# Kernel tuning notes

Measured on AMD Instinct MI355X. Metric: run time of the kernel, lower is better.

## Reference

```python
import jax, jax.numpy as jnp
import numpy as np
import math

N_HEADS = 16
ROPE_THETA = 10000.0


def _rope_cos_sin(seqlen, head_dim, theta=ROPE_THETA):
    # freqs_cis = polar(1, outer(t, 1/theta^(2i/d))) -> return cos, sin parts
    inv = 1.0 / (theta ** (jnp.arange(0, head_dim, 2, dtype=jnp.float32) / head_dim))
    t = jnp.arange(seqlen, dtype=jnp.float32)
    freqs = t[:, None] * inv[None, :]          # [S, hd/2]
    return jnp.cos(freqs), jnp.sin(freqs)


def _apply_rope(x, cos, sin):
    # x: [B, S, H, hd]; treat consecutive pairs as complex, rotate by e^{i*freq}
    B, S, H, hd = x.shape
    x2 = x.astype(jnp.float32).reshape(B, S, H, hd // 2, 2)
    xr, xi = x2[..., 0], x2[..., 1]
    c = cos[None, :, None, :]
    s = sin[None, :, None, :]
    out_r = xr * c - xi * s
    out_i = xr * s + xi * c
    return jnp.stack([out_r, out_i], axis=-1).reshape(B, S, H, hd).astype(x.dtype)


def setup_inputs() -> dict:
    key = jax.random.key(0)
    ks = jax.random.split(key, 5)
    dim = 2048
    B, S = 2, 2048
    scale = 1.0 / math.sqrt(dim)
    x = jax.random.normal(ks[0], (B, S, dim), dtype=jnp.float32)
    wq = jax.random.normal(ks[1], (dim, dim), dtype=jnp.float32) * scale
    wk = jax.random.normal(ks[2], (dim, dim), dtype=jnp.float32) * scale
    wv = jax.random.normal(ks[3], (dim, dim), dtype=jnp.float32) * scale
    wo = jax.random.normal(ks[4], (dim, dim), dtype=jnp.float32) * scale
    return {"x": x, "wq": wq, "wk": wk, "wv": wv, "wo": wo}


def reference(x, wq, wk, wv, wo):
    B, S, D = x.shape
    H = N_HEADS
    hd = D // H
    # nn.Linear(bias=False): y = x @ W.T
    q = (x @ wq.T).reshape(B, S, H, hd)
    k = (x @ wk.T).reshape(B, S, H, hd)
    v = (x @ wv.T).reshape(B, S, H, hd)
    cos, sin = _rope_cos_sin(S, hd)
    q = _apply_rope(q, cos, sin)
    k = _apply_rope(k, cos, sin)
    attn = jnp.einsum('bthd,bThd->bhtT', q, k) / jnp.sqrt(jnp.float32(hd))
    attn = jax.nn.softmax(attn, axis=-1)
    out = jnp.einsum('bhtT,bThd->bthd', attn, v).reshape(B, S, D)
    return out @ wo.T
```

## Files before the change

### kernel.cpp

```cpp
#include <hip/hip_runtime.h>
#include <math.h>

typedef unsigned short u16;
typedef __bf16 bf16x8 __attribute__((ext_vector_type(8)));
typedef short s16x4 __attribute__((ext_vector_type(4)));
typedef short s16x8 __attribute__((ext_vector_type(8)));
typedef float f32x4 __attribute__((ext_vector_type(4)));

#define B_ 2
#define S_ 2048
#define D_ 2048
#define H_ 16
#define HD_ 128
#define M_ 4096
#define N3_ 6144

#define AS1(p) ((__attribute__((address_space(1))) void*)(void*)(p))
#define AS3(p) ((__attribute__((address_space(3))) void*)(p))
#define GLD16(g, l) __builtin_amdgcn_global_load_lds(AS1(g), AS3(l), 16, 0, 0)

__device__ __forceinline__ u16 f2bf(float f) {
  unsigned u = __float_as_uint(f);
  return (u16)((u + 0x7FFFu + ((u >> 16) & 1u)) >> 16);
}
__device__ __forceinline__ float bf2f(u16 v) {
  return __uint_as_float(((unsigned)v) << 16);
}

__global__ void prep_k(const float* __restrict__ x, const float* __restrict__ wq,
                       const float* __restrict__ wk, const float* __restrict__ wv,
                       const float* __restrict__ wo, u16* __restrict__ xb,
                       u16* __restrict__ wqkvb, u16* __restrict__ wob,
                       float2* __restrict__ tab) {
  int idx = blockIdx.x * 256 + threadIdx.x;
  if (idx < 6291456) {
    const float* src;
    u16* dst;
    if (idx < 2097152) {
      src = x + (size_t)idx * 4;
      dst = xb + (size_t)idx * 4;
    } else if (idx < 5242880) {
      int ow = idx - 2097152;
      const float* w = ow < 1048576 ? wq : (ow < 2097152 ? wk : wv);
      int wo_off = ow & 1048575;
      src = w + (size_t)wo_off * 4;
      dst = wqkvb + (size_t)ow * 4;
    } else {
      int ow = idx - 5242880;
      src = wo + (size_t)ow * 4;
      dst = wob + (size_t)ow * 4;
    }
    float4 v = *(const float4*)src;
    ushort4 o;
    o.x = f2bf(v.x); o.y = f2bf(v.y); o.z = f2bf(v.z); o.w = f2bf(v.w);
    *(ushort4*)dst = o;
  } else {
    int t = idx - 6291456;
    int s = t >> 6, i = t & 63;
    double inv = exp2(-(double)i * (13.287712379549449 / 64.0));
    double fr = (double)s * inv;
    double sv, cv;
    sincos(fr, &sv, &cv);
    tab[t] = make_float2((float)cv, (float)sv);
  }
}

template <typename OT>
__global__ __launch_bounds__(256) void gemm_bt_k(const u16* __restrict__ A,
                                                 const u16* __restrict__ B,
                                                 OT* __restrict__ C,
                                                 int M, int N, int K) {
  __shared__ alignas(16) u16 As[128 * 32];
  __shared__ alignas(16) u16 Bs[128 * 32];
  const int tid = threadIdx.x;
  const int wave = tid >> 6, lane = tid & 63;
  const int quad = lane >> 4, l16 = lane & 15;
  const int m0 = blockIdx.y * 128, n0 = blockIdx.x * 128;
  const int wm = (wave >> 1) * 64, wn = (wave & 1) * 64;
  const u16* Ag = A + (size_t)m0 * K;
  const u16* Bg = B + (size_t)n0 * K;
  f32x4 acc[4][4] = {};
  const int c0 = tid, c1 = tid + 256;
  const int r0 = c0 >> 2, k0b = (c0 & 3) * 8;
  const int r1 = c1 >> 2, k1b = (c1 & 3) * 8;
  u16* la0 = As + (size_t)(wave * 64) * 8;
  u16* la1 = As + (size_t)(256 + wave * 64) * 8;
  u16* lb0 = Bs + (size_t)(wave * 64) * 8;
  u16* lb1 = Bs + (size_t)(256 + wave * 64) * 8;
  for (int kt = 0; kt < K; kt += 32) {
    GLD16(Ag + (size_t)r0 * K + kt + k0b, la0);
    GLD16(Ag + (size_t)r1 * K + kt + k1b, la1);
    GLD16(Bg + (size_t)r0 * K + kt + k0b, lb0);
    GLD16(Bg + (size_t)r1 * K + kt + k1b, lb1);
    __syncthreads();
    bf16x8 af[4], bfr[4];
#pragma unroll
    for (int i = 0; i < 4; ++i)
      af[i] = *(const bf16x8*)&As[(wm + i * 16 + l16) * 32 + quad * 8];
#pragma unroll
    for (int j = 0; j < 4; ++j)
      bfr[j] = *(const bf16x8*)&Bs[(wn + j * 16 + l16) * 32 + quad * 8];
#pragma unroll
    for (int i = 0; i < 4; ++i)
#pragma unroll
      for (int j = 0; j < 4; ++j)
        acc[i][j] = __builtin_amdgcn_mfma_f32_16x16x32_bf16(af[i], bfr[j], acc[i][j], 0, 0, 0);
    __syncthreads();
  }
#pragma unroll
  for (int i = 0; i < 4; ++i) {
#pragma unroll
    for (int j = 0; j < 4; ++j) {
      int n = n0 + wn + j * 16 + l16;
#pragma unroll
      for (int r = 0; r < 4; ++r) {
        int m = m0 + wm + i * 16 + quad * 4 + r;
        if constexpr (sizeof(OT) == 4)
          C[(size_t)m * N + n] = acc[i][j][r];
        else
          C[(size_t)m * N + n] = f2bf(acc[i][j][r]);
      }
    }
  }
}

__global__ void rv_k(const u16* __restrict__ qkv, const float2* __restrict__ tab,
                     u16* __restrict__ Qr, u16* __restrict__ Kr, u16* __restrict__ Vp) {
  int idx = blockIdx.x * 256 + threadIdx.x;
  if (idx < 4194304) {
    int m = idx >> 10;
    int h = (idx >> 6) & 15;
    int i = idx & 63;
    int s = m & (S_ - 1);
    int b = m >> 11;
    float2 cs = tab[(s << 6) | i];
    const u16* qp = qkv + (size_t)m * N3_ + h * HD_ + 2 * i;
    ushort2 qv = *(const ushort2*)qp;
    ushort2 kv = *(const ushort2*)(qp + D_);
    float qr = bf2f(qv.x), qi = bf2f(qv.y);
    float kr = bf2f(kv.x), ki = bf2f(kv.y);
    ushort2 qo, ko;
    qo.x = f2bf(qr * cs.x - qi * cs.y);
    qo.y = f2bf(qr * cs.y + qi * cs.x);
    ko.x = f2bf(kr * cs.x - ki * cs.y);
    ko.y = f2bf(kr * cs.y + ki * cs.x);
    size_t o = ((size_t)(b * H_ + h) * S_ + s) * HD_ + 2 * i;
    *(ushort2*)(Qr + o) = qo;
    *(ushort2*)(Kr + o) = ko;
  } else {
    int u = idx - 4194304;
    int bh = u >> 16, t = u & 65535;
    int b = bh >> 4, h = bh & 15;
    int d = t & 127, g = t >> 7;
    const u16* src = qkv + ((size_t)(b * S_ + 4 * g)) * N3_ + 2 * D_ + h * HD_ + d;
    ushort4 o;
    o.x = src[0];
    o.y = src[N3_];
    o.z = src[2 * N3_];
    o.w = src[3 * N3_];
    *(ushort4*)(Vp + (size_t)bh * S_ * HD_ + (size_t)t * 4) = o;
  }
}

#if __has_builtin(__builtin_amdgcn_mfma_f32_16x16x16bf16_1k)
#define HAS_MFMA16 1
#endif

__global__ __launch_bounds__(256, 3) void flash_k(const u16* __restrict__ Q,
                                                  const u16* __restrict__ Kc,
                                                  const u16* __restrict__ Vp,
                                                  float* __restrict__ Op0,
                                                  float* __restrict__ Op1,
                                                  float* __restrict__ lbuf) {
  __shared__ alignas(16) u16 sm[16384];
  u16* Ks = sm;
  u16* Vs = sm + 8192;
  const int tid = threadIdx.x;
  const int wave = tid >> 6, lane = tid & 63;
  const int quad = lane >> 4, l16 = lane & 15;
  const int qt = blockIdx.x;
  const int bh = blockIdx.y & 31, split = blockIdx.y >> 5;
  const int b = bh >> 4, h = bh & 15;

  bf16x8 qf[2][4];
#pragma unroll
  for (int half = 0; half < 2; ++half) {
#pragma unroll
    for (int i = 0; i < 4; ++i) {
      int c = i * 256 + tid, row = c >> 4, jl = c & 15;
      int gj = (jl & 8) | ((jl ^ row) & 7);
      GLD16(Q + ((size_t)bh * S_ + qt * 128 + half * 64 + row) * HD_ + gj * 8,
            sm + (size_t)(i * 256 + wave * 64) * 8);
    }
    __syncthreads();
    if ((wave >> 1) == half) {
      int wrow = (wave & 1) * 32;
#pragma unroll
      for (int qs = 0; qs < 2; ++qs) {
        int row = wrow + qs * 16 + l16;
#pragma unroll
        for (int dk = 0; dk < 4; ++dk) {
          int c = dk * 4 + quad, pj = (c & 8) | ((c ^ row) & 7);
          qf[qs][dk] = *(const bf16x8*)&sm[row * 128 + pj * 8];
        }
      }
    }
    __syncthreads();
  }

  f32x4 acco[2][8] = {};
  f32x4 accl[2] = {};
  const float SCL = 0.08838834764831845f * 1.4426950408889634f;
#ifdef HAS_MFMA16
  const s16x4 ones = {(short)0x3F80, (short)0x3F80, (short)0x3F80, (short)0x3F80};
#else
  union { s16x8 s; bf16x8 b; } onesu;
  onesu.s = (s16x8){(short)0x3F80, (short)0x3F80, (short)0x3F80, (short)0x3F80,
                    (short)0x3F80, (short)0x3F80, (short)0x3F80, (short)0x3F80};
#endif

  const int kt0 = split * 16, kt1 = kt0 + 16;
#pragma unroll 1
  for (int kt = kt0; kt < kt1; ++kt) {
#pragma unroll
    for (int i = 0; i < 4; ++i) {
      int c = i * 256 + tid, row = c >> 4, jl = c & 15;
      int gj = (jl & 8) | ((jl ^ row) & 7);
      GLD16(Kc + ((size_t)bh * S_ + kt * 64 + row) * HD_ + gj * 8,
            Ks + (size_t)(i * 256 + wave * 64) * 8);
    }
    const u16* vg = Vp + (size_t)bh * S_ * HD_ + (size_t)kt * 8192;
#pragma unroll
    for (int i = 0; i < 4; ++i)
      GLD16(vg + (size_t)(i * 256 + tid) * 8, Vs + (size_t)(i * 256 + wave * 64) * 8);
    __syncthreads();

    f32x4 sc[2][4] = {};
#pragma unroll
    for (int k4 = 0; k4 < 4; ++k4) {
      int row = k4 * 16 + l16;
#pragma unroll
      for (int dk = 0; dk < 4; ++dk) {
        int c = dk * 4 + quad, pj = (c & 8) | ((c ^ row) & 7);
        bf16x8 kf = *(const bf16x8*)&Ks[row * 128 + pj * 8];
        sc[0][k4] = __builtin_amdgcn_mfma_f32_16x16x32_bf16(kf, qf[0][dk], sc[0][k4], 0, 0, 0);
        sc[1][k4] = __builtin_amdgcn_mfma_f32_16x16x32_bf16(kf, qf[1][dk], sc[1][k4], 0, 0, 0);
      }
    }

#ifdef HAS_MFMA16
    s16x4 ap[2][4];
#else
    bf16x8 ap[2][4];
#endif
#pragma unroll
    for (int qs = 0; qs < 2; ++qs) {
#pragma unroll
      for (int k4 = 0; k4 < 4; ++k4) {
        f32x4 s = sc[qs][k4];
        u16 p0 = f2bf(__builtin_amdgcn_exp2f(s[0] * SCL));
        u16 p1 = f2bf(__builtin_amdgcn_exp2f(s[1] * SCL));
        u16 p2 = f2bf(__builtin_amdgcn_exp2f(s[2] * SCL));
        u16 p3 = f2bf(__builtin_amdgcn_exp2f(s[3] * SCL));
#ifdef HAS_MFMA16
        ap[qs][k4] = (s16x4){(short)p0, (short)p1, (short)p2, (short)p3};
#else
        union { s16x8 s8; bf16x8 b8; } u;
        u.s8 = (s16x8){(short)p0, (short)p1, (short)p2, (short)p3, 0, 0, 0, 0};
        ap[qs][k4] = u.b8;
#endif
      }
    }

#pragma unroll
    for (int ck = 0; ck < 4; ++ck) {
      int vbase = (ck * 4 + quad) * 512 + l16 * 4;
#pragma unroll
      for (int df = 0; df < 8; ++df) {
        s16x4 bv = *(const s16x4*)&Vs[vbase + df * 64];
#ifdef HAS_MFMA16
        acco[0][df] = __builtin_amdgcn_mfma_f32_16x16x16bf16_1k(ap[0][ck], bv, acco[0][df], 0, 0, 0);
        acco[1][df] = __builtin_amdgcn_mfma_f32_16x16x16bf16_1k(ap[1][ck], bv, acco[1][df], 0, 0, 0);
#else
        union { s16x8 s8; bf16x8 b8; } vb;
        vb.s8 = (s16x8){bv[0], bv[1], bv[2], bv[3], 0, 0, 0, 0};
        acco[0][df] = __builtin_amdgcn_mfma_f32_16x16x32_bf16(ap[0][ck], vb.b8, acco[0][df], 0, 0, 0);
        acco[1][df] = __builtin_amdgcn_mfma_f32_16x16x32_bf16(ap[1][ck], vb.b8, acco[1][df], 0, 0, 0);
#endif
      }
#ifdef HAS_MFMA16
      accl[0] = __builtin_amdgcn_mfma_f32_16x16x16bf16_1k(ones, ap[0][ck], accl[0], 0, 0, 0);
      accl[1] = __builtin_amdgcn_mfma_f32_16x16x16bf16_1k(ones, ap[1][ck], accl[1], 0, 0, 0);
#else
      accl[0] = __builtin_amdgcn_mfma_f32_16x16x32_bf16(onesu.b, ap[0][ck], accl[0], 0, 0, 0);
      accl[1] = __builtin_amdgcn_mfma_f32_16x16x32_bf16(onesu.b, ap[1][ck], accl[1], 0, 0, 0);
#endif
    }
    __syncthreads();
  }

  float* op = split ? Op1 : Op0;
#pragma unroll
  for (int qs = 0; qs < 2; ++qs) {
    int rowb = qt * 128 + wave * 32 + qs * 16 + quad * 4;
#pragma unroll
    for (int df = 0; df < 8; ++df) {
      int col = h * HD_ + df * 16 + l16;
#pragma unroll
      for (int r = 0; r < 4; ++r)
        op[((size_t)(b * S_ + rowb + r)) * D_ + col] = acco[qs][df][r];
    }
    if (quad == 0)
      lbuf[(size_t)split * 65536 + bh * 2048 + qt * 128 + wave * 32 + qs * 16 + l16] =
          accl[qs][0];
  }
}

__global__ void merge_k(const float* __restrict__ Op0, const float* __restrict__ Op1,
                        const float* __restrict__ lbuf, u16* __restrict__ Ob) {
  int i4 = blockIdx.x * 256 + threadIdx.x;
  int row = i4 >> 9, col4 = i4 & 511;
  int b = row >> 11, s = row & 2047, h4 = col4 >> 5;
  int bh = (b << 4) | h4;
  float l = lbuf[bh * 2048 + s] + lbuf[65536 + bh * 2048 + s];
  float inv = 1.0f / l;
  float4 a = ((const float4*)Op0)[i4];
  float4 c = ((const float4*)Op1)[i4];
  ushort4 o;
  o.x = f2bf((a.x + c.x) * inv);
  o.y = f2bf((a.y + c.y) * inv);
  o.z = f2bf((a.z + c.z) * inv);
  o.w = f2bf((a.w + c.w) * inv);
  ((ushort4*)Ob)[i4] = o;
}

extern "C" void kernel_launch(void* const* d_in, const int* in_sizes, int n_in,
                              void* d_out, int out_size, void* d_ws, size_t ws_size,
                              hipStream_t stream) {
  const float* x  = (const float*)d_in[0];
  const float* wq = (const float*)d_in[1];
  const float* wk = (const float*)d_in[2];
  const float* wv = (const float*)d_in[3];
  const float* wo = (const float*)d_in[4];

  size_t off = 0;
  char* ws = (char*)d_ws;
  u16* xb    = (u16*)(ws + off); off += (size_t)M_ * D_ * 2;
  u16* wqkvb = (u16*)(ws + off); off += (size_t)3 * D_ * D_ * 2;
  u16* wob   = (u16*)(ws + off); off += (size_t)D_ * D_ * 2;
  u16* qkv   = (u16*)(ws + off); off += (size_t)M_ * N3_ * 2;
  u16* Qr    = (u16*)(ws + off); off += (size_t)M_ * D_ * 2;
  u16* Kr    = (u16*)(ws + off); off += (size_t)M_ * D_ * 2;
  u16* Vp    = (u16*)(ws + off); off += (size_t)M_ * D_ * 2;
  float2* tab = (float2*)(ws + off); off += (size_t)S_ * 64 * sizeof(float2);
  float* Op0  = (float*)ws;
  u16*   Ob   = qkv;
  float* Op1  = (float*)(ws + ((size_t)64 << 20));
  float* lbuf = (float*)tab;
  if (off > ws_size) return;

  prep_k<<<25088, 256, 0, stream>>>(x, wq, wk, wv, wo, xb, wqkvb, wob, tab);
  gemm_bt_k<u16><<<dim3(N3_ / 128, M_ / 128), 256, 0, stream>>>(xb, wqkvb, qkv, M_, N3_, D_);
  rv_k<<<24576, 256, 0, stream>>>(qkv, tab, Qr, Kr, Vp);
  flash_k<<<dim3(S_ / 128, 64), 256, 0, stream>>>(Qr, Kr, Vp, Op0, Op1, lbuf);
  merge_k<<<(M_ * D_ / 4) / 256, 256, 0, stream>>>(Op0, Op1, lbuf, Ob);
  gemm_bt_k<float><<<dim3(D_ / 128, M_ / 128), 256, 0, stream>>>(Ob, wob, (float*)d_out, M_, D_, D_);
}
```

Baseline: 462.7 us.

## Fuse RoPE and V repack into QKV GEMM epilogue; drop flash split-K merge

The QKV GEMM now applies RoPE to Q and K and writes V in its packed layout directly from the accumulators, using a lane shuffle to pair neighbouring elements. This removes the separate rv_k pass and the bf16 qkv intermediate round trip through memory. Flash attention no longer splits the key range in two. Each block processes all 32 key tiles and normalizes in the epilogue, writing bf16 output directly, which removes merge_k and the two fp32 partial output buffers. The trade-off is half as many flash blocks (512 instead of 1024), so there is less parallelism to fill the GPU. The GEMM epilogue also adds scattered table loads.

```diff
diff --git a/kernel.cpp b/kernel.cpp
--- a/kernel.cpp
+++ b/kernel.cpp
@@ -62,6 +62,93 @@
     double sv, cv;
     sincos(fr, &sv, &cv);
     tab[t] = make_float2((float)cv, (float)sv);
+  }
+}
+
+__global__ __launch_bounds__(256) void gemm_qkv_k(const u16* __restrict__ A,
+                                                  const u16* __restrict__ B,
+                                                  const float2* __restrict__ tab,
+                                                  u16* __restrict__ Qr,
+                                                  u16* __restrict__ Kr,
+                                                  u16* __restrict__ Vp) {
+  __shared__ alignas(16) u16 As[128 * 32];
+  __shared__ alignas(16) u16 Bs[128 * 32];
+  const int K = D_;
+  const int tid = threadIdx.x;
+  const int wave = tid >> 6, lane = tid & 63;
+  const int quad = lane >> 4, l16 = lane & 15;
+  const int m0 = blockIdx.y * 128, n0 = blockIdx.x * 128;
+  const int wm = (wave >> 1) * 64, wn = (wave & 1) * 64;
+  const u16* Ag = A + (size_t)m0 * K;
+  const u16* Bg = B + (size_t)n0 * K;
+  f32x4 acc[4][4] = {};
+  const int c0 = tid, c1 = tid + 256;
+  const int r0 = c0 >> 2, k0b = (c0 & 3) * 8;
+  const int r1 = c1 >> 2, k1b = (c1 & 3) * 8;
+  u16* la0 = As + (size_t)(wave * 64) * 8;
+  u16* la1 = As + (size_t)(256 + wave * 64) * 8;
+  u16* lb0 = Bs + (size_t)(wave * 64) * 8;
+  u16* lb1 = Bs + (size_t)(256 + wave * 64) * 8;
+  for (int kt = 0; kt < K; kt += 32) {
+    GLD16(Ag + (size_t)r0 * K + kt + k0b, la0);
+    GLD16(Ag + (size_t)r1 * K + kt + k1b, la1);
+    GLD16(Bg + (size_t)r0 * K + kt + k0b, lb0);
+    GLD16(Bg + (size_t)r1 * K + kt + k1b, lb1);
+    __syncthreads();
+    bf16x8 af[4], bfr[4];
+#pragma unroll
+    for (int i = 0; i < 4; ++i)
+      af[i] = *(const bf16x8*)&As[(wm + i * 16 + l16) * 32 + quad * 8];
+#pragma unroll
+    for (int j = 0; j < 4; ++j)
+      bfr[j] = *(const bf16x8*)&Bs[(wn + j * 16 + l16) * 32 + quad * 8];
+#pragma unroll
+    for (int i = 0; i < 4; ++i)
+#pragma unroll
+      for (int j = 0; j < 4; ++j)
+        acc[i][j] = __builtin_amdgcn_mfma_f32_16x16x32_bf16(af[i], bfr[j], acc[i][j], 0, 0, 0);
+    __syncthreads();
+  }
+
+  const int region = n0 >> 11;
+  const int h = (n0 >> 7) & 15;
+  if (region < 2) {
+    u16* dst = region ? Kr : Qr;
+#pragma unroll
+    for (int i = 0; i < 4; ++i) {
+#pragma unroll
+      for (int j = 0; j < 4; ++j) {
+        int d = wn + j * 16 + l16;
+        int ii = d >> 1;
+        float sgn = (d & 1) ? 1.f : -1.f;
+#pragma unroll
+        for (int r = 0; r < 4; ++r) {
+          int m = m0 + wm + i * 16 + quad * 4 + r;
+          int s = m & (S_ - 1), b = m >> 11;
+          float2 cs = tab[(s << 6) + ii];
+          float v = acc[i][j][r];
+          float p = __shfl_xor(v, 1);
+          float o = v * cs.x + sgn * p * cs.y;
+          dst[((size_t)((b << 4) + h) * S_ + s) * HD_ + d] = f2bf(o);
+        }
+      }
+    }
+  } else {
+#pragma unroll
+    for (int i = 0; i < 4; ++i) {
+#pragma unroll
+      for (int j = 0; j < 4; ++j) {
+        int d = wn + j * 16 + l16;
+        int rowb = m0 + wm + i * 16 + quad * 4;
+        int b = rowb >> 11, sl = rowb & (S_ - 1);
+        ushort4 o;
+        o.x = f2bf(acc[i][j][0]);
+        o.y = f2bf(acc[i][j][1]);
+        o.z = f2bf(acc[i][j][2]);
+        o.w = f2bf(acc[i][j][3]);
+        *(ushort4*)(Vp + (size_t)((b << 4) + h) * S_ * HD_ + (size_t)(sl >> 2) * 512 + d * 4) = o;
+      }
+    }
   }
 }
 
@@ -124,44 +211,6 @@
   }
 }
 
-__global__ void rv_k(const u16* __restrict__ qkv, const float2* __restrict__ tab,
-                     u16* __restrict__ Qr, u16* __restrict__ Kr, u16* __restrict__ Vp) {
-  int idx = blockIdx.x * 256 + threadIdx.x;
-  if (idx < 4194304) {
-    int m = idx >> 10;
-    int h = (idx >> 6) & 15;
-    int i = idx & 63;
-    int s = m & (S_ - 1);
-    int b = m >> 11;
-    float2 cs = tab[(s << 6) | i];
-    const u16* qp = qkv + (size_t)m * N3_ + h * HD_ + 2 * i;
-    ushort2 qv = *(const ushort2*)qp;
-    ushort2 kv = *(const ushort2*)(qp + D_);
-    float qr = bf2f(qv.x), qi = bf2f(qv.y);
-    float kr = bf2f(kv.x), ki = bf2f(kv.y);
-    ushort2 qo, ko;
-    qo.x = f2bf(qr * cs.x - qi * cs.y);
-    qo.y = f2bf(qr * cs.y + qi * cs.x);
-    ko.x = f2bf(kr * cs.x - ki * cs.y);
-    ko.y = f2bf(kr * cs.y + ki * cs.x);
-    size_t o = ((size_t)(b * H_ + h) * S_ + s) * HD_ + 2 * i;
-    *(ushort2*)(Qr + o) = qo;
-    *(ushort2*)(Kr + o) = ko;
-  } else {
-    int u = idx - 4194304;
-    int bh = u >> 16, t = u & 65535;
-    int b = bh >> 4, h = bh & 15;
-    int d = t & 127, g = t >> 7;
-    const u16* src = qkv + ((size_t)(b * S_ + 4 * g)) * N3_ + 2 * D_ + h * HD_ + d;
-    ushort4 o;
-    o.x = src[0];
-    o.y = src[N3_];
-    o.z = src[2 * N3_];
-    o.w = src[3 * N3_];
-    *(ushort4*)(Vp + (size_t)bh * S_ * HD_ + (size_t)t * 4) = o;
-  }
-}
-
 #if __has_builtin(__builtin_amdgcn_mfma_f32_16x16x16bf16_1k)
 #define HAS_MFMA16 1
 #endif
@@ -169,17 +218,14 @@
 __global__ __launch_bounds__(256, 3) void flash_k(const u16* __restrict__ Q,
                                                   const u16* __restrict__ Kc,
                                                   const u16* __restrict__ Vp,
-                                                  float* __restrict__ Op0,
-                                                  float* __restrict__ Op1,
-                                                  float* __restrict__ lbuf) {
+                                                  u16* __restrict__ O) {
   __shared__ alignas(16) u16 sm[16384];
   u16* Ks = sm;
   u16* Vs = sm + 8192;
   const int tid = threadIdx.x;
   const int wave = tid >> 6, lane = tid & 63;
   const int quad = lane >> 4, l16 = lane & 15;
-  const int qt = blockIdx.x;
-  const int bh = blockIdx.y & 31, split = blockIdx.y >> 5;
+  const int qt = blockIdx.x, bh = blockIdx.y;
   const int b = bh >> 4, h = bh & 15;
 
   bf16x8 qf[2][4];
@@ -219,9 +265,8 @@
                     (short)0x3F80, (short)0x3F80, (short)0x3F80, (short)0x3F80};
 #endif
 
-  const int kt0 = split * 16, kt1 = kt0 + 16;
 #pragma unroll 1
-  for (int kt = kt0; kt < kt1; ++kt) {
+  for (int kt = 0; kt < 32; ++kt) {
 #pragma unroll
     for (int i = 0; i < 4; ++i) {
       int c = i * 256 + tid, row = c >> 4, jl = c & 15;
@@ -299,39 +344,21 @@
     __syncthreads();
   }
 
-  float* op = split ? Op1 : Op0;
 #pragma unroll
   for (int qs = 0; qs < 2; ++qs) {
+    float lv = accl[qs][0];
+    float linv[4];
+#pragma unroll
+    for (int r = 0; r < 4; ++r) linv[r] = 1.0f / __shfl(lv, quad * 4 + r);
     int rowb = qt * 128 + wave * 32 + qs * 16 + quad * 4;
 #pragma unroll
     for (int df = 0; df < 8; ++df) {
       int col = h * HD_ + df * 16 + l16;
 #pragma unroll
       for (int r = 0; r < 4; ++r)
-        op[((size_t)(b * S_ + rowb + r)) * D_ + col] = acco[qs][df][r];
-    }
-    if (quad == 0)
-      lbuf[(size_t)split * 65536 + bh * 2048 + qt * 128 + wave * 32 + qs * 16 + l16] =
-          accl[qs][0];
-  }
-}
-
-__global__ void merge_k(const float* __restrict__ Op0, const float* __restrict__ Op1,
-                        const float* __restrict__ lbuf, u16* __restrict__ Ob) {
-  int i4 = blockIdx.x * 256 + threadIdx.x;
-  int row = i4 >> 9, col4 = i4 & 511;
-  int b = row >> 11, s = row & 2047, h4 = col4 >> 5;
-  int bh = (b << 4) | h4;
-  float l = lbuf[bh * 2048 + s] + lbuf[65536 + bh * 2048 + s];
-  float inv = 1.0f / l;
-  float4 a = ((const float4*)Op0)[i4];
-  float4 c = ((const float4*)Op1)[i4];
-  ushort4 o;
-  o.x = f2bf((a.x + c.x) * inv);
-  o.y = f2bf((a.y + c.y) * inv);
-  o.z = f2bf((a.z + c.z) * inv);
-  o.w = f2bf((a.w + c.w) * inv);
-  ((ushort4*)Ob)[i4] = o;
+        O[((size_t)(b * S_ + rowb + r)) * D_ + col] = f2bf(acco[qs][df][r] * linv[r]);
+    }
+  }
 }
 
 extern "C" void kernel_launch(void* const* d_in, const int* in_sizes, int n_in,
@@ -348,21 +375,15 @@
   u16* xb    = (u16*)(ws + off); off += (size_t)M_ * D_ * 2;
   u16* wqkvb = (u16*)(ws + off); off += (size_t)3 * D_ * D_ * 2;
   u16* wob   = (u16*)(ws + off); off += (size_t)D_ * D_ * 2;
-  u16* qkv   = (u16*)(ws + off); off += (size_t)M_ * N3_ * 2;
   u16* Qr    = (u16*)(ws + off); off += (size_t)M_ * D_ * 2;
   u16* Kr    = (u16*)(ws + off); off += (size_t)M_ * D_ * 2;
   u16* Vp    = (u16*)(ws + off); off += (size_t)M_ * D_ * 2;
   float2* tab = (float2*)(ws + off); off += (size_t)S_ * 64 * sizeof(float2);
-  float* Op0  = (float*)ws;
-  u16*   Ob   = qkv;
-  float* Op1  = (float*)(ws + ((size_t)64 << 20));
-  float* lbuf = (float*)tab;
+  u16* Ob = xb;
   if (off > ws_size) return;
 
   prep_k<<<25088, 256, 0, stream>>>(x, wq, wk, wv, wo, xb, wqkvb, wob, tab);
-  gemm_bt_k<u16><<<dim3(N3_ / 128, M_ / 128), 256, 0, stream>>>(xb, wqkvb, qkv, M_, N3_, D_);
-  rv_k<<<24576, 256, 0, stream>>>(qkv, tab, Qr, Kr, Vp);
-  flash_k<<<dim3(S_ / 128, 64), 256, 0, stream>>>(Qr, Kr, Vp, Op0, Op1, lbuf);
-  merge_k<<<(M_ * D_ / 4) / 256, 256, 0, stream>>>(Op0, Op1, lbuf, Ob);
+  gemm_qkv_k<<<dim3(N3_ / 128, M_ / 128), 256, 0, stream>>>(xb, wqkvb, tab, Qr, Kr, Vp);
+  flash_k<<<dim3(S_ / 128, B_ * H_), 256, 0, stream>>>(Qr, Kr, Vp, Ob);
   gemm_bt_k<float><<<dim3(D_ / 128, M_ / 128), 256, 0, stream>>>(Ob, wob, (float*)d_out, M_, D_, D_);
 }
```

Measured after the change: 444.5 us. 3.9% less time.
